# Kernel tuning notes

Hardware: AMD Instinct MI355X
Metric: run time of the kernel (lower is better)

Reference implementation:

```python
import jax, jax.numpy as jnp
import numpy as np

B, N, W = 4, 16384, 4          # batch, npoints, point feature width (xyz + intensity)
M, K = 512, 32                  # nsample keypoints, neighbors per keypoint
DIL = 2.0
NK = int(K * DIL)               # dilated candidate pool
KG = 8                          # knn size inside DGCNN edge-convs
C3 = 256


def _fps(xyz, m):
    """Farthest point sampling. xyz: (B,N,3) -> indices (B,m)."""
    Bb, Nn, _ = xyz.shape
    def step(carry, _):
        mind, cur = carry
        p = jnp.take_along_axis(xyz, cur[:, None, None], axis=1)  # (B,1,3)
        d = jnp.sum((xyz - p) ** 2, axis=-1)                       # (B,N)
        mind = jnp.minimum(mind, d)
        nxt = jnp.argmax(mind, axis=-1).astype(jnp.int32)
        return (mind, nxt), cur
    init = (jnp.full((Bb, Nn), 1e10, xyz.dtype), jnp.zeros((Bb,), jnp.int32))
    _, idx = jax.lax.scan(step, init, None, length=m)
    return jnp.transpose(idx)  # (B,m)


def _edge_conv(x, w, g, b, kg):
    """Dynamic-graph edge conv. x: (G,P,C) -> (G,P,D). Feature = cat(x_j-x_i, x_i)."""
    sq = jnp.sum(x * x, axis=-1)
    d2 = sq[:, :, None] + sq[:, None, :] - 2.0 * jnp.einsum('gpc,gqc->gpq', x, x)
    _, idx = jax.lax.top_k(-d2, kg)                                   # (G,P,kg)
    xj = jnp.take_along_axis(x[:, None], idx[..., None], axis=2)      # (G,P,kg,C)
    ef = jnp.concatenate([xj - x[:, :, None, :],
                          jnp.broadcast_to(x[:, :, None, :], xj.shape)], axis=-1)
    h = jnp.einsum('gpkc,cd->gpkd', ef, w)
    h = jax.nn.relu(g * h + b)  # BN (inference, unit running stats) + ReLU
    return jnp.max(h, axis=2)   # max over graph neighbors


def setup_inputs() -> dict:
    key = jax.random.key(0)
    ks = jax.random.split(key, 12)
    s = 0.05
    inp = {
        'x': jax.random.normal(ks[0], (B, N, W), jnp.float32),
        'rand_idx': jax.random.randint(ks[1], (K,), 0, NK),
        # DGCNN edge-conv params
        'w_e1': jax.random.normal(ks[2], (24, 64), jnp.float32) * s,
        'g1': jnp.ones((64,), jnp.float32), 'b1': jnp.zeros((64,), jnp.float32),
        'w_e2': jax.random.normal(ks[3], (128, C3), jnp.float32) * s,
        'g2': jnp.ones((C3,), jnp.float32), 'b2': jnp.zeros((C3,), jnp.float32),
        # saliency MLP (1x1 conv1d stacks)
        'w_m1': jax.random.normal(ks[4], (C3, C3), jnp.float32) * s,
        'bm1': jnp.zeros((C3,), jnp.float32),
        'gm1': jnp.ones((C3,), jnp.float32), 'bbm1': jnp.zeros((C3,), jnp.float32),
        'w_m2': jax.random.normal(ks[5], (C3, C3), jnp.float32) * s,
        'bm2': jnp.zeros((C3,), jnp.float32),
        'gm2': jnp.ones((C3,), jnp.float32), 'bbm2': jnp.zeros((C3,), jnp.float32),
        'w_m3': jax.random.normal(ks[6], (C3, 1), jnp.float32) * s,
        'bm3': jnp.zeros((1,), jnp.float32),
    }
    return inp


def reference(x, rand_idx, w_e1, g1, b1, w_e2, g2, b2,
              w_m1, bm1, gm1, bbm1, w_m2, bm2, gm2, bbm2, w_m3, bm3):
    rand_idx = rand_idx.astype(jnp.int32)
    # ---- FPS keypoint sampling ----
    node_idx = _fps(x[:, :, :3], M)                                   # (B,M)
    node = jnp.take_along_axis(x, node_idx[:, :, None], axis=1)       # (B,M,W)
    # ---- random dilation encoding: nk-NN then random k of them ----
    nxyz, pxyz = node[:, :, :3], x[:, :, :3]
    d2 = (jnp.sum(nxyz * nxyz, -1)[:, :, None] + jnp.sum(pxyz * pxyz, -1)[:, None, :]
          - 2.0 * jnp.einsum('bmc,bnc->bmn', nxyz, pxyz))             # (B,M,N)
    _, nn = jax.lax.top_k(-d2, NK)                                    # (B,M,NK)
    sel = nn[:, :, rand_idx]                                          # (B,M,K)
    neigh = jnp.take_along_axis(x[:, None], sel[..., None], axis=2)   # (B,M,K,W)
    rel = neigh[..., :3] - nxyz[:, :, None, :]
    dist = jnp.linalg.norm(rel, axis=-1, keepdims=True)
    node_rep = jnp.broadcast_to(node[:, :, None, :], neigh.shape)
    cluster = jnp.concatenate([node_rep, neigh, rel, dist], axis=-1)  # (B,M,K,12)
    random_cluster = jnp.transpose(cluster, (0, 3, 1, 2))             # (B,12,M,K)
    random_xyz = neigh[..., :3]                                       # (B,M,K,3)
    # ---- DGCNN embedding per cluster ----
    g = cluster.reshape(B * M, K, 12)
    h = _edge_conv(g, w_e1, g1, b1, KG)                               # (BM,K,64)
    h = _edge_conv(h, w_e2, g2, b2, KG)                               # (BM,K,256)
    emb = jnp.transpose(h.reshape(B, M, K, C3), (0, 3, 1, 2))         # (B,256,M,K)
    # ---- attention-weighted pooling ----
    x1 = jnp.max(emb, axis=1)                                         # (B,M,K)
    aw = jax.nn.softmax(x1, axis=-1)
    keypoints = jnp.einsum('bmk,bmkc->bcm', aw, random_xyz)           # (B,3,M)
    afm = emb * aw[:, None]                                           # (B,256,M,K)
    gcf = jnp.sum(afm, axis=-1)                                       # (B,256,M)
    # ---- saliency uncertainty MLP ----
    h = jax.nn.relu(gm1[None, :, None] * (jnp.einsum('bcm,cd->bdm', gcf, w_m1)
                                          + bm1[None, :, None]) + bbm1[None, :, None])
    h = jax.nn.relu(gm2[None, :, None] * (jnp.einsum('bcm,cd->bdm', h, w_m2)
                                          + bm2[None, :, None]) + bbm2[None, :, None])
    s = jnp.einsum('bcm,cd->bdm', h, w_m3) + bm3[None, :, None]       # (B,1,M)
    sal = jax.nn.softplus(s)[:, 0, :] + 0.001                         # (B,M)
    return keypoints, sal, random_cluster, afm
```

## Files before the change

kernel.cpp:

```cpp
#include <hip/hip_runtime.h>
#include <cstdint>

#define Bn 4
#define Nn 16384
#define Mn 512
#define Kn 32

#define O_SAL 6144
#define O_RC  8192
#define O_AFM 794624

__device__ __forceinline__ unsigned fkey(float f) {
  unsigned b = __float_as_uint(f);
  return (b & 0x80000000u) ? ~b : (b | 0x80000000u);
}

__device__ __forceinline__ unsigned long long dkey(double d) {
  unsigned long long b = (unsigned long long)__double_as_longlong(d);
  return (b & 0x8000000000000000ull) ? ~b : (b | 0x8000000000000000ull);
}

__global__ __launch_bounds__(256) void sq_kernel(const float* __restrict__ x,
                                                 float* __restrict__ sqp) {
#pragma clang fp contract(off)
  int i = blockIdx.x * 256 + threadIdx.x;
  float4 v = ((const float4*)x)[i];
  float qx = v.x * v.x;
  float qy = v.y * v.y;
  float qz = v.z * v.z;
  sqp[i] = (qx + qy) + qz;
}

template <int CTRL>
__device__ __forceinline__ float dppmaxf(float v) {
  int m = __builtin_amdgcn_update_dpp(__float_as_int(v), __float_as_int(v),
                                      CTRL, 0xf, 0xf, false);
  return fmaxf(v, __int_as_float(m));
}

__global__ __launch_bounds__(1024)
__attribute__((amdgpu_waves_per_eu(4, 4)))
void fps_kernel(const float* __restrict__ x, float* __restrict__ node) {
#pragma clang fp contract(off)
  const int b = blockIdx.x;
  const int t = threadIdx.x;
  const float4* xb = (const float4*)(x + (size_t)b * Nn * 4);
  float px[16], py[16], pz[16], mind[16];
  const int base = t * 16;
#pragma unroll
  for (int i = 0; i < 16; ++i) {
    float4 v = xb[base + i];
    px[i] = v.x; py[i] = v.y; pz[i] = v.z;
    mind[i] = 1e10f;
  }
  __shared__ __align__(16) unsigned long long kkey[2][16];
  float cx, cy, cz;
  {
    float4 v = xb[0];
    cx = v.x; cy = v.y; cz = v.z;
    if (t == 0) ((float4*)node)[b * Mn] = v;
  }
  for (int s = 1; s < Mn; ++s) {
#pragma unroll
    for (int i = 0; i < 16; ++i) {
      float dx = px[i] - cx;
      float dy = py[i] - cy;
      float dz = pz[i] - cz;
      float qx = dx * dx;
      float qy = dy * dy;
      float qz = dz * dz;
      float d = (qx + qy) + qz;
      mind[i] = fminf(mind[i], d);
    }
    float a0 = fmaxf(mind[0], mind[1]);
    float a1 = fmaxf(mind[2], mind[3]);
    float a2 = fmaxf(mind[4], mind[5]);
    float a3 = fmaxf(mind[6], mind[7]);
    float a4 = fmaxf(mind[8], mind[9]);
    float a5 = fmaxf(mind[10], mind[11]);
    float a6 = fmaxf(mind[12], mind[13]);
    float a7 = fmaxf(mind[14], mind[15]);
    float b0 = fmaxf(a0, a1);
    float b1 = fmaxf(a2, a3);
    float b2 = fmaxf(a4, a5);
    float b3 = fmaxf(a6, a7);
    float bv = fmaxf(fmaxf(b0, b1), fmaxf(b2, b3));
    int isel = 0;
#pragma unroll
    for (int i = 15; i >= 0; --i)
      if (mind[i] == bv) isel = i;
    float r = bv;
    r = dppmaxf<0x111>(r);
    r = dppmaxf<0x112>(r);
    r = dppmaxf<0x114>(r);
    r = dppmaxf<0x118>(r);
    r = dppmaxf<0x142>(r);
    r = dppmaxf<0x143>(r);
    float wmax = __int_as_float(__builtin_amdgcn_readlane(__float_as_int(r), 63));
    unsigned long long ball = __ballot(bv == wmax);
    int wl = __ffsll(ball) - 1;
    int widx = __builtin_amdgcn_readlane(base + isel, wl);
    if ((t & 63) == 0) {
      kkey[s & 1][t >> 6] =
          ((unsigned long long)(__float_as_uint(wmax) | 0x80000000u) << 32) |
          (unsigned)(~widx);
    }
    __syncthreads();
    {
      unsigned long long kk = kkey[s & 1][t & 15];
#pragma unroll
      for (int off = 1; off < 16; off <<= 1) {
        unsigned long long ok = __shfl_xor(kk, off, 16);
        kk = ok > kk ? ok : kk;
      }
      int wi = __builtin_amdgcn_readfirstlane((int)(~(unsigned)(kk & 0xFFFFFFFFu)));
      float4 nv = xb[wi];
      cx = nv.x; cy = nv.y; cz = nv.z;
      if (t == 0) ((float4*)node)[b * Mn + s] = nv;
    }
  }
}

__global__ __launch_bounds__(256) void knn_kernel(const float* __restrict__ x,
                                                  const float* __restrict__ node,
                                                  const float* __restrict__ sqp,
                                                  const int* __restrict__ rand_idx,
                                                  int* __restrict__ sel) {
#pragma clang fp contract(off)
  const int bm = blockIdx.x;
  const int b = bm >> 9;
  const int t = threadIdx.x;
  const float4* xb = (const float4*)(x + (size_t)b * Nn * 4);
  const float* sq_b = sqp + b * Nn;
  float4 nd = ((const float4*)node)[bm];
  const float nx = nd.x, ny = nd.y, nz = nd.z;
  const float sqmf = (nx * nx + ny * ny) + nz * nz;
  unsigned key[64];
#pragma unroll
  for (int i = 0; i < 64; ++i) {
    int n = t + (i << 8);
    float4 v = xb[n];
    float dot = nx * v.x;
    dot = __builtin_fmaf(ny, v.y, dot);
    dot = __builtin_fmaf(nz, v.z, dot);
    float d2 = (sqmf + sq_b[n]) - 2.0f * dot;
    key[i] = fkey(d2);
  }
  __shared__ unsigned hist[256];
  __shared__ unsigned gsum[16];
  __shared__ unsigned sh_prefix;
  __shared__ int sh_r;
  unsigned prefix = 0, pmask = 0;
  int r = 95;
  for (int shift = 24; shift >= 0; shift -= 8) {
    hist[t] = 0;
    __syncthreads();
#pragma unroll
    for (int i = 0; i < 64; ++i) {
      if ((key[i] & pmask) == prefix) atomicAdd(&hist[(key[i] >> shift) & 255], 1u);
    }
    __syncthreads();
    if (t < 16) {
      unsigned ssum = 0;
#pragma unroll
      for (int j = 0; j < 16; ++j) ssum += hist[t * 16 + j];
      gsum[t] = ssum;
    }
    __syncthreads();
    if (t == 0) {
      int rr = r;
      unsigned g = 0;
      for (unsigned j = 0; j < 16; ++j) {
        int c = (int)gsum[j];
        if (rr < c) { g = j; break; }
        rr -= c;
      }
      unsigned bin = g * 16;
      for (unsigned j = 0; j < 16; ++j) {
        int c = (int)hist[g * 16 + j];
        if (rr < c) { bin = g * 16 + j; break; }
        rr -= c;
      }
      sh_prefix = prefix | (bin << shift);
      sh_r = rr;
    }
    __syncthreads();
    prefix = sh_prefix;
    r = sh_r;
    pmask |= (0xFFu << shift);
  }
  const unsigned T = prefix;
  __shared__ int cnt;
  __shared__ unsigned long long karr[128];
  if (t == 0) cnt = 0;
  __syncthreads();
#pragma unroll
  for (int i = 0; i < 64; ++i) {
    if (key[i] <= T) {
      int pos = atomicAdd(&cnt, 1);
      if (pos < 128) {
        unsigned n = (unsigned)(t + (i << 8));
        karr[pos] = ((unsigned long long)key[i] << 32) | n;
      }
    }
  }
  __syncthreads();
  const int nc = cnt < 128 ? cnt : 128;
  if (t < 128 && t >= nc) karr[t] = ~0ull;
  for (int k = 2; k <= 128; k <<= 1) {
    for (int j = k >> 1; j > 0; j >>= 1) {
      __syncthreads();
      if (t < 64) {
        int i = ((t & ~(j - 1)) << 1) | (t & (j - 1));
        int ip = i | j;
        unsigned long long ka = karr[i], kb = karr[ip];
        bool asc = ((i & k) == 0);
        if ((ka > kb) == asc) { karr[i] = kb; karr[ip] = ka; }
      }
    }
  }
  __syncthreads();
  if (t < 32) {
    int ri = rand_idx[t];
    sel[bm * 32 + t] = (int)(unsigned)(karr[ri] & 0xFFFFFFFFu);
  }
}

__global__ __launch_bounds__(256) void group_kernel(
    const float* __restrict__ x, const float* __restrict__ node,
    const int* __restrict__ sel, const float* __restrict__ w_e1,
    const float* __restrict__ g1, const float* __restrict__ b1,
    const float* __restrict__ w_e2, const float* __restrict__ g2,
    const float* __restrict__ b2, float* __restrict__ out,
    float* __restrict__ gcf) {
#pragma clang fp contract(off)
  const int bm = blockIdx.x;
  const int b = bm >> 9;
  const int m = bm & 511;
  const int t = threadIdx.x;

  __shared__ float cl[32][13];
  __shared__ float h1t[64][36];
  __shared__ float h1p[32][68];
  __shared__ unsigned char nbr[32][8];
  __shared__ double sqs[32];
  __shared__ float part[4][32];
  __shared__ float aws[32];
  __shared__ union U {
    struct {
      unsigned long long keys[32][32];
      float we_a[12][64];
      float we_d[12][64];
      float a1[32][65];
      float cd1[32][65];
    } s;
    float a2[32 * 256];
  } u;

  const float4* xb = (const float4*)(x + (size_t)b * Nn * 4);
  const float4 ndv = ((const float4*)node)[bm];

  if (t < 32) {
    int n = sel[bm * 32 + t];
    float4 v = xb[n];
    float rx = v.x - ndv.x;
    float ry = v.y - ndv.y;
    float rz = v.z - ndv.z;
    float ds = (rx * rx + ry * ry) + rz * rz;
    ds = __fsqrt_rn(ds);
    cl[t][0] = ndv.x; cl[t][1] = ndv.y; cl[t][2] = ndv.z; cl[t][3] = ndv.w;
    cl[t][4] = v.x;   cl[t][5] = v.y;   cl[t][6] = v.z;   cl[t][7] = v.w;
    cl[t][8] = rx;    cl[t][9] = ry;    cl[t][10] = rz;   cl[t][11] = ds;
  }
  for (int i = t; i < 768; i += 256) {
    int row = i >> 6, d = i & 63;
    float wa = w_e1[row * 64 + d];
    float wb = w_e1[(row + 12) * 64 + d];
    u.s.we_a[row][d] = wa;
    u.s.we_d[row][d] = wb - wa;
  }
  __syncthreads();

  for (int i = t; i < 384; i += 256) {
    int c = i >> 5, p = i & 31;
    out[O_RC + (((size_t)(b * 12 + c) * 512) + m) * 32 + p] = cl[p][c];
  }
  if (t < 32) {
    double q[12];
#pragma unroll
    for (int c = 0; c < 12; ++c) {
      double cv = (double)cl[t][c];
      q[c] = cv * cv;
    }
    double s01 = q[0] + q[1];
    double s23 = q[2] + q[3];
    double s45 = q[4] + q[5];
    double s67 = q[6] + q[7];
    double s = (s01 + s23) + (s45 + s67);
    s = s + q[8];
    s = s + q[9];
    s = s + q[10];
    s = s + q[11];
    sqs[t] = s;
  }
  __syncthreads();

  {
    int p = t >> 3, q0 = (t & 7) << 2;
#pragma unroll
    for (int qq = 0; qq < 4; ++qq) {
      int q = q0 + qq;
      double dot = 0.0;
#pragma unroll
      for (int c = 0; c < 12; ++c)
        dot = dot + (double)cl[p][c] * (double)cl[q][c];
      double d2 = (sqs[p] + sqs[q]) - 2.0 * dot;
      u.s.keys[p][q] = dkey(d2);
    }
  }
  __syncthreads();

  {
    int p = t >> 3, s8 = t & 7;
    unsigned long long kq0 = u.s.keys[p][s8];
    unsigned long long kq1 = u.s.keys[p][s8 + 8];
    unsigned long long kq2 = u.s.keys[p][s8 + 16];
    unsigned long long kq3 = u.s.keys[p][s8 + 24];
    int r0 = 0, r1 = 0, r2 = 0, r3 = 0;
#pragma unroll
    for (int j = 0; j < 32; ++j) {
      int jj = (j + p) & 31;
      unsigned long long kj = u.s.keys[p][jj];
      r0 += (kj < kq0 || (kj == kq0 && jj < s8));
      r1 += (kj < kq1 || (kj == kq1 && jj < s8 + 8));
      r2 += (kj < kq2 || (kj == kq2 && jj < s8 + 16));
      r3 += (kj < kq3 || (kj == kq3 && jj < s8 + 24));
    }
    if (r0 < 8) nbr[p][r0] = (unsigned char)s8;
    if (r1 < 8) nbr[p][r1] = (unsigned char)(s8 + 8);
    if (r2 < 8) nbr[p][r2] = (unsigned char)(s8 + 16);
    if (r3 < 8) nbr[p][r3] = (unsigned char)(s8 + 24);
  }
  {
    int d = t & 63, pg = (t >> 6) << 3;
#pragma unroll
    for (int pp = 0; pp < 8; ++pp) {
      int p = pg + pp;
      float aA = 0.f, aD = 0.f;
#pragma unroll
      for (int c = 0; c < 12; ++c) {
        float xv = cl[p][c];
        aA = fmaf(xv, u.s.we_a[c][d], aA);
        aD = fmaf(xv, u.s.we_d[c][d], aD);
      }
      u.s.a1[p][d] = aA;
      u.s.cd1[p][d] = aD;
    }
  }
  __syncthreads();

  {
    int d = t & 63, pg = (t >> 6) << 3;
    float g1v = g1[d], b1v = b1[d];
#pragma unroll
    for (int pp = 0; pp < 8; ++pp) {
      int p = pg + pp;
      float cd = u.s.cd1[p][d];
      float hm = -1e30f;
#pragma unroll
      for (int k = 0; k < 8; ++k) {
        int j = nbr[p][k];
        float hv = fmaf(g1v, u.s.a1[j][d] + cd, b1v);
        hv = fmaxf(hv, 0.f);
        hm = fmaxf(hm, hv);
      }
      h1t[d][p] = hm;
      h1p[p][d] = hm;
    }
  }
  __syncthreads();

  if (t < 32) {
    double r[8];
#pragma unroll
    for (int j = 0; j < 8; ++j) {
      double hv = (double)h1p[t][j];
      r[j] = hv * hv;
    }
#pragma unroll
    for (int blk = 1; blk < 8; ++blk) {
#pragma unroll
      for (int j = 0; j < 8; ++j) {
        double hv = (double)h1p[t][blk * 8 + j];
        r[j] = r[j] + hv * hv;
      }
    }
    double s01 = r[0] + r[1];
    double s23 = r[2] + r[3];
    double s45 = r[4] + r[5];
    double s67 = r[6] + r[7];
    sqs[t] = (s01 + s23) + (s45 + s67);
  }
  __syncthreads();

  {
    int p = t >> 3, q0 = (t & 7) << 2;
    const float4* rp = (const float4*)&h1p[p][0];
    for (int qq = 0; qq < 4; ++qq) {
      int q = q0 + qq;
      const float4* rq = (const float4*)&h1p[q][0];
      double dot = 0.0;
#pragma unroll
      for (int c4 = 0; c4 < 16; ++c4) {
        float4 av = rp[c4];
        float4 bv = rq[c4];
        dot = dot + (double)av.x * (double)bv.x;
        dot = dot + (double)av.y * (double)bv.y;
        dot = dot + (double)av.z * (double)bv.z;
        dot = dot + (double)av.w * (double)bv.w;
      }
      double d2 = (sqs[p] + sqs[q]) - 2.0 * dot;
      u.s.keys[p][q] = dkey(d2);
    }
  }
  __syncthreads();

  {
    int p = t >> 3, s8 = t & 7;
    unsigned long long kq0 = u.s.keys[p][s8];
    unsigned long long kq1 = u.s.keys[p][s8 + 8];
    unsigned long long kq2 = u.s.keys[p][s8 + 16];
    unsigned long long kq3 = u.s.keys[p][s8 + 24];
    int r0 = 0, r1 = 0, r2 = 0, r3 = 0;
#pragma unroll
    for (int j = 0; j < 32; ++j) {
      int jj = (j + p) & 31;
      unsigned long long kj = u.s.keys[p][jj];
      r0 += (kj < kq0 || (kj == kq0 && jj < s8));
      r1 += (kj < kq1 || (kj == kq1 && jj < s8 + 8));
      r2 += (kj < kq2 || (kj == kq2 && jj < s8 + 16));
      r3 += (kj < kq3 || (kj == kq3 && jj < s8 + 24));
    }
    if (r0 < 8) nbr[p][r0] = (unsigned char)s8;
    if (r1 < 8) nbr[p][r1] = (unsigned char)(s8 + 8);
    if (r2 < 8) nbr[p][r2] = (unsigned char)(s8 + 16);
    if (r3 < 8) nbr[p][r3] = (unsigned char)(s8 + 24);
  }
  __syncthreads();

  float accD[32];
  float embv[32];
  {
    float accA[32];
#pragma unroll
    for (int p = 0; p < 32; ++p) { accA[p] = 0.f; accD[p] = 0.f; }
    for (int c = 0; c < 64; ++c) {
      float wt = w_e2[c * 256 + t];
      float wb = w_e2[(c + 64) * 256 + t];
      float wd = wb - wt;
      const float4* row = (const float4*)&h1t[c][0];
#pragma unroll
      for (int p4 = 0; p4 < 8; ++p4) {
        float4 hv = row[p4];
        accA[4 * p4 + 0] = fmaf(hv.x, wt, accA[4 * p4 + 0]);
        accA[4 * p4 + 1] = fmaf(hv.y, wt, accA[4 * p4 + 1]);
        accA[4 * p4 + 2] = fmaf(hv.z, wt, accA[4 * p4 + 2]);
        accA[4 * p4 + 3] = fmaf(hv.w, wt, accA[4 * p4 + 3]);
        accD[4 * p4 + 0] = fmaf(hv.x, wd, accD[4 * p4 + 0]);
        accD[4 * p4 + 1] = fmaf(hv.y, wd, accD[4 * p4 + 1]);
        accD[4 * p4 + 2] = fmaf(hv.z, wd, accD[4 * p4 + 2]);
        accD[4 * p4 + 3] = fmaf(hv.w, wd, accD[4 * p4 + 3]);
      }
    }
#pragma unroll
    for (int p = 0; p < 32; ++p) u.a2[p * 256 + t] = accA[p];
  }
  __syncthreads();
  {
    float g2v = g2[t], b2v = b2[t];
#pragma unroll
    for (int p = 0; p < 32; ++p) {
      float cd = accD[p];
      float e = -1e30f;
#pragma unroll
      for (int k = 0; k < 8; ++k) {
        int j = nbr[p][k];
        float hv = fmaf(g2v, u.a2[j * 256 + t] + cd, b2v);
        hv = fmaxf(hv, 0.f);
        e = fmaxf(e, hv);
      }
      embv[p] = e;
    }
  }

#pragma unroll
  for (int p = 0; p < 32; ++p) {
    float v = embv[p];
#pragma unroll
    for (int off = 32; off > 0; off >>= 1) v = fmaxf(v, __shfl_xor(v, off));
    if ((t & 63) == 0) part[t >> 6][p] = v;
  }
  __syncthreads();

  if (t < 32) {
    float x1 = fmaxf(fmaxf(part[0][t], part[1][t]), fmaxf(part[2][t], part[3][t]));
    float mx = x1;
#pragma unroll
    for (int off = 16; off > 0; off >>= 1) mx = fmaxf(mx, __shfl_xor(mx, off));
    float ex = expf(x1 - mx);
    float sm = ex;
#pragma unroll
    for (int off = 16; off > 0; off >>= 1) sm += __shfl_xor(sm, off);
    float aw = ex / sm;
    aws[t] = aw;
#pragma unroll
    for (int c = 0; c < 3; ++c) {
      float kv = aw * cl[t][4 + c];
#pragma unroll
      for (int off = 16; off > 0; off >>= 1) kv += __shfl_xor(kv, off);
      if (t == 0) out[((size_t)(b * 3 + c)) * 512 + m] = kv;
    }
  }
  __syncthreads();

  {
    float gsum = 0.f;
    size_t abase = (size_t)O_AFM + (((size_t)(b * 256 + t)) * 512 + m) * 32;
    float4* ap = (float4*)(out + abase);
#pragma unroll
    for (int p4 = 0; p4 < 8; ++p4) {
      float4 o;
      o.x = embv[4 * p4 + 0] * aws[4 * p4 + 0];
      o.y = embv[4 * p4 + 1] * aws[4 * p4 + 1];
      o.z = embv[4 * p4 + 2] * aws[4 * p4 + 2];
      o.w = embv[4 * p4 + 3] * aws[4 * p4 + 3];
      gsum += o.x; gsum += o.y; gsum += o.z; gsum += o.w;
      ap[p4] = o;
    }
    gcf[((size_t)(b * 256 + t)) * 512 + m] = gsum;
  }
}

__global__ __launch_bounds__(256) void mlp_kernel(
    const float* __restrict__ gcf, const float* __restrict__ w_m1,
    const float* __restrict__ bm1, const float* __restrict__ gm1,
    const float* __restrict__ bbm1, const float* __restrict__ w_m2,
    const float* __restrict__ bm2, const float* __restrict__ gm2,
    const float* __restrict__ bbm2, const float* __restrict__ w_m3,
    const float* __restrict__ bm3, float* __restrict__ out) {
  const int blk = blockIdx.x;
  const int b = blk >> 4;
  const int m0 = (blk & 15) << 5;
  const int t = threadIdx.x;
  __shared__ float sbuf[256 * 36];

#pragma unroll
  for (int i = 0; i < 32; ++i) {
    int c = (t >> 5) + (i << 3);
    int j = t & 31;
    sbuf[c * 36 + j] = gcf[((size_t)(b * 256 + c)) * 512 + m0 + j];
  }
  __syncthreads();

  float acc[32];
#pragma unroll
  for (int j = 0; j < 32; ++j) acc[j] = 0.f;
  for (int c = 0; c < 256; ++c) {
    float wv = w_m1[c * 256 + t];
    const float4* row = (const float4*)&sbuf[c * 36];
#pragma unroll
    for (int j4 = 0; j4 < 8; ++j4) {
      float4 g4 = row[j4];
      acc[4 * j4 + 0] = fmaf(g4.x, wv, acc[4 * j4 + 0]);
      acc[4 * j4 + 1] = fmaf(g4.y, wv, acc[4 * j4 + 1]);
      acc[4 * j4 + 2] = fmaf(g4.z, wv, acc[4 * j4 + 2]);
      acc[4 * j4 + 3] = fmaf(g4.w, wv, acc[4 * j4 + 3]);
    }
  }
  float y[32];
  {
    float gv = gm1[t], bv = bm1[t], bbv = bbm1[t];
#pragma unroll
    for (int j = 0; j < 32; ++j) y[j] = fmaxf(fmaf(gv, acc[j] + bv, bbv), 0.f);
  }
  __syncthreads();
#pragma unroll
  for (int j = 0; j < 32; ++j) sbuf[t * 36 + j] = y[j];
  __syncthreads();

#pragma unroll
  for (int j = 0; j < 32; ++j) acc[j] = 0.f;
  for (int c = 0; c < 256; ++c) {
    float wv = w_m2[c * 256 + t];
    const float4* row = (const float4*)&sbuf[c * 36];
#pragma unroll
    for (int j4 = 0; j4 < 8; ++j4) {
      float4 g4 = row[j4];
      acc[4 * j4 + 0] = fmaf(g4.x, wv, acc[4 * j4 + 0]);
      acc[4 * j4 + 1] = fmaf(g4.y, wv, acc[4 * j4 + 1]);
      acc[4 * j4 + 2] = fmaf(g4.z, wv, acc[4 * j4 + 2]);
      acc[4 * j4 + 3] = fmaf(g4.w, wv, acc[4 * j4 + 3]);
    }
  }
  {
    float gv = gm2[t], bv = bm2[t], bbv = bbm2[t];
#pragma unroll
    for (int j = 0; j < 32; ++j) y[j] = fmaxf(fmaf(gv, acc[j] + bv, bbv), 0.f);
  }
  __syncthreads();
  {
    float w3v = w_m3[t];
#pragma unroll
    for (int j = 0; j < 32; ++j) sbuf[t * 36 + j] = y[j] * w3v;
  }
  __syncthreads();
  if (t < 32) {
    float s = 0.f;
    for (int d = 0; d < 256; ++d) s += sbuf[d * 36 + t];
    s += bm3[0];
    float sal = log1pf(expf(-fabsf(s))) + fmaxf(s, 0.f) + 0.001f;
    out[O_SAL + (size_t)b * 512 + m0 + t] = sal;
  }
}

extern "C" void kernel_launch(void* const* d_in, const int* in_sizes, int n_in,
                              void* d_out, int out_size, void* d_ws, size_t ws_size,
                              hipStream_t stream) {
  (void)in_sizes; (void)n_in; (void)out_size; (void)ws_size;
  const float* x = (const float*)d_in[0];
  const int* rand_idx = (const int*)d_in[1];
  const float* w_e1 = (const float*)d_in[2];
  const float* g1 = (const float*)d_in[3];
  const float* b1 = (const float*)d_in[4];
  const float* w_e2 = (const float*)d_in[5];
  const float* g2 = (const float*)d_in[6];
  const float* b2 = (const float*)d_in[7];
  const float* w_m1 = (const float*)d_in[8];
  const float* bm1 = (const float*)d_in[9];
  const float* gm1 = (const float*)d_in[10];
  const float* bbm1 = (const float*)d_in[11];
  const float* w_m2 = (const float*)d_in[12];
  const float* bm2 = (const float*)d_in[13];
  const float* gm2 = (const float*)d_in[14];
  const float* bbm2 = (const float*)d_in[15];
  const float* w_m3 = (const float*)d_in[16];
  const float* bm3 = (const float*)d_in[17];
  float* out = (float*)d_out;
  char* ws = (char*)d_ws;

  float* node = (float*)ws;
  float* sqp = (float*)(ws + 32768);
  int* sel = (int*)(ws + 32768 + 262144);
  float* gcf = (float*)(ws + 32768 + 262144 + 262144);

  sq_kernel<<<256, 256, 0, stream>>>(x, sqp);
  fps_kernel<<<Bn, 1024, 0, stream>>>(x, node);
  knn_kernel<<<Bn * Mn, 256, 0, stream>>>(x, node, sqp, rand_idx, sel);
  group_kernel<<<Bn * Mn, 256, 0, stream>>>(x, node, sel, w_e1, g1, b1, w_e2,
                                            g2, b2, out, gcf);
  mlp_kernel<<<64, 256, 0, stream>>>(gcf, w_m1, bm1, gm1, bbm1, w_m2, bm2, gm2,
                                     bbm2, w_m3, bm3, out);
}
```

Before: 1.551 ms.

## Fuse FPS and KNN into a persistent kernel with flag-based producer-consumer overlap

Merges the sequential farthest-point-sampling kernel and the KNN selection kernel into one 512-block launch. Blocks 0-3 run FPS and publish progress every 8 sampled points through release-stored flags. The remaining blocks poll those flags with acquire loads, then run radix-select KNN for each newly ready keypoint. The goal is to hide KNN behind the long serial FPS loop and drop a kernel launch. The cost is spin-waiting, a dependence on the FPS blocks actually being resident so the pollers cannot deadlock, flags that alias the gcf workspace, and an added topk8 helper that nothing calls.

```diff
diff --git a/kernel.cpp b/kernel.cpp
--- a/kernel.cpp
+++ b/kernel.cpp
@@ -21,9 +21,11 @@
 }
 
 __global__ __launch_bounds__(256) void sq_kernel(const float* __restrict__ x,
-                                                 float* __restrict__ sqp) {
+                                                 float* __restrict__ sqp,
+                                                 unsigned long long* __restrict__ flags) {
 #pragma clang fp contract(off)
   int i = blockIdx.x * 256 + threadIdx.x;
+  if (blockIdx.x == 0 && threadIdx.x < 4) flags[threadIdx.x * 8] = 0ull;
   float4 v = ((const float4*)x)[i];
   float qx = v.x * v.x;
   float qy = v.y * v.y;
@@ -40,190 +42,228 @@
 
 __global__ __launch_bounds__(1024)
 __attribute__((amdgpu_waves_per_eu(4, 4)))
-void fps_kernel(const float* __restrict__ x, float* __restrict__ node) {
+void fused_fps_knn(const float* __restrict__ x, float* __restrict__ node,
+                   const float* __restrict__ sqp,
+                   const int* __restrict__ rand_idx, int* __restrict__ sel,
+                   unsigned long long* __restrict__ flags) {
 #pragma clang fp contract(off)
-  const int b = blockIdx.x;
   const int t = threadIdx.x;
-  const float4* xb = (const float4*)(x + (size_t)b * Nn * 4);
-  float px[16], py[16], pz[16], mind[16];
-  const int base = t * 16;
-#pragma unroll
-  for (int i = 0; i < 16; ++i) {
-    float4 v = xb[base + i];
-    px[i] = v.x; py[i] = v.y; pz[i] = v.z;
-    mind[i] = 1e10f;
-  }
   __shared__ __align__(16) unsigned long long kkey[2][16];
-  float cx, cy, cz;
-  {
-    float4 v = xb[0];
-    cx = v.x; cy = v.y; cz = v.z;
-    if (t == 0) ((float4*)node)[b * Mn] = v;
-  }
-  for (int s = 1; s < Mn; ++s) {
-#pragma unroll
-    for (int i = 0; i < 16; ++i) {
-      float dx = px[i] - cx;
-      float dy = py[i] - cy;
-      float dz = pz[i] - cz;
-      float qx = dx * dx;
-      float qy = dy * dy;
-      float qz = dz * dz;
-      float d = (qx + qy) + qz;
-      mind[i] = fminf(mind[i], d);
-    }
-    float a0 = fmaxf(mind[0], mind[1]);
-    float a1 = fmaxf(mind[2], mind[3]);
-    float a2 = fmaxf(mind[4], mind[5]);
-    float a3 = fmaxf(mind[6], mind[7]);
-    float a4 = fmaxf(mind[8], mind[9]);
-    float a5 = fmaxf(mind[10], mind[11]);
-    float a6 = fmaxf(mind[12], mind[13]);
-    float a7 = fmaxf(mind[14], mind[15]);
-    float b0 = fmaxf(a0, a1);
-    float b1 = fmaxf(a2, a3);
-    float b2 = fmaxf(a4, a5);
-    float b3 = fmaxf(a6, a7);
-    float bv = fmaxf(fmaxf(b0, b1), fmaxf(b2, b3));
-    int isel = 0;
-#pragma unroll
-    for (int i = 15; i >= 0; --i)
-      if (mind[i] == bv) isel = i;
-    float r = bv;
-    r = dppmaxf<0x111>(r);
-    r = dppmaxf<0x112>(r);
-    r = dppmaxf<0x114>(r);
-    r = dppmaxf<0x118>(r);
-    r = dppmaxf<0x142>(r);
-    r = dppmaxf<0x143>(r);
-    float wmax = __int_as_float(__builtin_amdgcn_readlane(__float_as_int(r), 63));
-    unsigned long long ball = __ballot(bv == wmax);
-    int wl = __ffsll(ball) - 1;
-    int widx = __builtin_amdgcn_readlane(base + isel, wl);
-    if ((t & 63) == 0) {
-      kkey[s & 1][t >> 6] =
-          ((unsigned long long)(__float_as_uint(wmax) | 0x80000000u) << 32) |
-          (unsigned)(~widx);
-    }
-    __syncthreads();
-    {
-      unsigned long long kk = kkey[s & 1][t & 15];
-#pragma unroll
-      for (int off = 1; off < 16; off <<= 1) {
-        unsigned long long ok = __shfl_xor(kk, off, 16);
-        kk = ok > kk ? ok : kk;
-      }
-      int wi = __builtin_amdgcn_readfirstlane((int)(~(unsigned)(kk & 0xFFFFFFFFu)));
-      float4 nv = xb[wi];
-      cx = nv.x; cy = nv.y; cz = nv.z;
-      if (t == 0) ((float4*)node)[b * Mn + s] = nv;
-    }
-  }
-}
-
-__global__ __launch_bounds__(256) void knn_kernel(const float* __restrict__ x,
-                                                  const float* __restrict__ node,
-                                                  const float* __restrict__ sqp,
-                                                  const int* __restrict__ rand_idx,
-                                                  int* __restrict__ sel) {
-#pragma clang fp contract(off)
-  const int bm = blockIdx.x;
-  const int b = bm >> 9;
-  const int t = threadIdx.x;
-  const float4* xb = (const float4*)(x + (size_t)b * Nn * 4);
-  const float* sq_b = sqp + b * Nn;
-  float4 nd = ((const float4*)node)[bm];
-  const float nx = nd.x, ny = nd.y, nz = nd.z;
-  const float sqmf = (nx * nx + ny * ny) + nz * nz;
-  unsigned key[64];
-#pragma unroll
-  for (int i = 0; i < 64; ++i) {
-    int n = t + (i << 8);
-    float4 v = xb[n];
-    float dot = nx * v.x;
-    dot = __builtin_fmaf(ny, v.y, dot);
-    dot = __builtin_fmaf(nz, v.z, dot);
-    float d2 = (sqmf + sq_b[n]) - 2.0f * dot;
-    key[i] = fkey(d2);
-  }
   __shared__ unsigned hist[256];
   __shared__ unsigned gsum[16];
   __shared__ unsigned sh_prefix;
   __shared__ int sh_r;
-  unsigned prefix = 0, pmask = 0;
-  int r = 95;
-  for (int shift = 24; shift >= 0; shift -= 8) {
-    hist[t] = 0;
-    __syncthreads();
-#pragma unroll
-    for (int i = 0; i < 64; ++i) {
-      if ((key[i] & pmask) == prefix) atomicAdd(&hist[(key[i] >> shift) & 255], 1u);
-    }
-    __syncthreads();
-    if (t < 16) {
-      unsigned ssum = 0;
-#pragma unroll
-      for (int j = 0; j < 16; ++j) ssum += hist[t * 16 + j];
-      gsum[t] = ssum;
-    }
-    __syncthreads();
-    if (t == 0) {
-      int rr = r;
-      unsigned g = 0;
-      for (unsigned j = 0; j < 16; ++j) {
-        int c = (int)gsum[j];
-        if (rr < c) { g = j; break; }
-        rr -= c;
-      }
-      unsigned bin = g * 16;
-      for (unsigned j = 0; j < 16; ++j) {
-        int c = (int)hist[g * 16 + j];
-        if (rr < c) { bin = g * 16 + j; break; }
-        rr -= c;
-      }
-      sh_prefix = prefix | (bin << shift);
-      sh_r = rr;
-    }
-    __syncthreads();
-    prefix = sh_prefix;
-    r = sh_r;
-    pmask |= (0xFFu << shift);
-  }
-  const unsigned T = prefix;
   __shared__ int cnt;
   __shared__ unsigned long long karr[128];
-  if (t == 0) cnt = 0;
-  __syncthreads();
-#pragma unroll
-  for (int i = 0; i < 64; ++i) {
-    if (key[i] <= T) {
-      int pos = atomicAdd(&cnt, 1);
-      if (pos < 128) {
-        unsigned n = (unsigned)(t + (i << 8));
-        karr[pos] = ((unsigned long long)key[i] << 32) | n;
-      }
-    }
-  }
-  __syncthreads();
-  const int nc = cnt < 128 ? cnt : 128;
-  if (t < 128 && t >= nc) karr[t] = ~0ull;
-  for (int k = 2; k <= 128; k <<= 1) {
-    for (int j = k >> 1; j > 0; j >>= 1) {
+
+  if (blockIdx.x < 4) {
+    const int b = blockIdx.x;
+    const float4* xb = (const float4*)(x + (size_t)b * Nn * 4);
+    float px[16], py[16], pz[16], mind[16];
+    const int base = t * 16;
+#pragma unroll
+    for (int i = 0; i < 16; ++i) {
+      float4 v = xb[base + i];
+      px[i] = v.x; py[i] = v.y; pz[i] = v.z;
+      mind[i] = 1e10f;
+    }
+    float cx, cy, cz;
+    {
+      float4 v = xb[0];
+      cx = v.x; cy = v.y; cz = v.z;
+      if (t == 0) ((float4*)node)[b * Mn] = v;
+    }
+    for (int s = 1; s < Mn; ++s) {
+#pragma unroll
+      for (int i = 0; i < 16; ++i) {
+        float dx = px[i] - cx;
+        float dy = py[i] - cy;
+        float dz = pz[i] - cz;
+        float qx = dx * dx;
+        float qy = dy * dy;
+        float qz = dz * dz;
+        float d = (qx + qy) + qz;
+        mind[i] = fminf(mind[i], d);
+      }
+      float a0 = fmaxf(mind[0], mind[1]);
+      float a1 = fmaxf(mind[2], mind[3]);
+      float a2 = fmaxf(mind[4], mind[5]);
+      float a3 = fmaxf(mind[6], mind[7]);
+      float a4 = fmaxf(mind[8], mind[9]);
+      float a5 = fmaxf(mind[10], mind[11]);
+      float a6 = fmaxf(mind[12], mind[13]);
+      float a7 = fmaxf(mind[14], mind[15]);
+      float b0 = fmaxf(a0, a1);
+      float b1 = fmaxf(a2, a3);
+      float b2 = fmaxf(a4, a5);
+      float b3 = fmaxf(a6, a7);
+      float bv = fmaxf(fmaxf(b0, b1), fmaxf(b2, b3));
+      int isel = 0;
+#pragma unroll
+      for (int i = 15; i >= 0; --i)
+        if (mind[i] == bv) isel = i;
+      float r = bv;
+      r = dppmaxf<0x111>(r);
+      r = dppmaxf<0x112>(r);
+      r = dppmaxf<0x114>(r);
+      r = dppmaxf<0x118>(r);
+      r = dppmaxf<0x142>(r);
+      r = dppmaxf<0x143>(r);
+      float wmax = __int_as_float(__builtin_amdgcn_readlane(__float_as_int(r), 63));
+      unsigned long long ball = __ballot(bv == wmax);
+      int wl = __ffsll(ball) - 1;
+      int widx = __builtin_amdgcn_readlane(base + isel, wl);
+      if ((t & 63) == 0) {
+        kkey[s & 1][t >> 6] =
+            ((unsigned long long)(__float_as_uint(wmax) | 0x80000000u) << 32) |
+            (unsigned)(~widx);
+      }
       __syncthreads();
-      if (t < 64) {
-        int i = ((t & ~(j - 1)) << 1) | (t & (j - 1));
-        int ip = i | j;
-        unsigned long long ka = karr[i], kb = karr[ip];
-        bool asc = ((i & k) == 0);
-        if ((ka > kb) == asc) { karr[i] = kb; karr[ip] = ka; }
-      }
-    }
-  }
-  __syncthreads();
-  if (t < 32) {
-    int ri = rand_idx[t];
-    sel[bm * 32 + t] = (int)(unsigned)(karr[ri] & 0xFFFFFFFFu);
-  }
+      {
+        unsigned long long kk = kkey[s & 1][t & 15];
+#pragma unroll
+        for (int off = 1; off < 16; off <<= 1) {
+          unsigned long long ok = __shfl_xor(kk, off, 16);
+          kk = ok > kk ? ok : kk;
+        }
+        int wi = __builtin_amdgcn_readfirstlane((int)(~(unsigned)(kk & 0xFFFFFFFFu)));
+        float4 nv = xb[wi];
+        cx = nv.x; cy = nv.y; cz = nv.z;
+        if (t == 0) ((float4*)node)[b * Mn + s] = nv;
+      }
+      if (((s & 7) == 7) && t == 0) {
+        __hip_atomic_store(&flags[b * 8], (unsigned long long)((s + 1) >> 3),
+                           __ATOMIC_RELEASE, __HIP_MEMORY_SCOPE_AGENT);
+      }
+    }
+  } else {
+    const int w = blockIdx.x - 4;
+    for (int j = w; j < Bn * Mn; j += 508) {
+      const int m = j >> 2;
+      const int bb = j & 3;
+      if (t == 0) {
+        unsigned long long need = (unsigned long long)((m >> 3) + 1);
+        while (__hip_atomic_load(&flags[bb * 8], __ATOMIC_ACQUIRE,
+                                 __HIP_MEMORY_SCOPE_AGENT) < need)
+          __builtin_amdgcn_s_sleep(8);
+      }
+      __syncthreads();
+
+      const int bm = bb * Mn + m;
+      const float4* xb = (const float4*)(x + (size_t)bb * Nn * 4);
+      const float* sq_b = sqp + bb * Nn;
+      float4 nd = ((const float4*)node)[bm];
+      const float nx = nd.x, ny = nd.y, nz = nd.z;
+      const float sqmf = (nx * nx + ny * ny) + nz * nz;
+      unsigned key[16];
+#pragma unroll
+      for (int i = 0; i < 16; ++i) {
+        int n = t + (i << 10);
+        float4 v = xb[n];
+        float dot = nx * v.x;
+        dot = __builtin_fmaf(ny, v.y, dot);
+        dot = __builtin_fmaf(nz, v.z, dot);
+        float d2 = (sqmf + sq_b[n]) - 2.0f * dot;
+        key[i] = fkey(d2);
+      }
+      unsigned prefix = 0, pmask = 0;
+      int r = 95;
+      for (int shift = 24; shift >= 0; shift -= 8) {
+        if (t < 256) hist[t] = 0;
+        __syncthreads();
+#pragma unroll
+        for (int i = 0; i < 16; ++i) {
+          if ((key[i] & pmask) == prefix)
+            atomicAdd(&hist[(key[i] >> shift) & 255], 1u);
+        }
+        __syncthreads();
+        if (t < 16) {
+          unsigned ssum = 0;
+#pragma unroll
+          for (int jj = 0; jj < 16; ++jj) ssum += hist[t * 16 + jj];
+          gsum[t] = ssum;
+        }
+        __syncthreads();
+        if (t == 0) {
+          int rr = r;
+          unsigned g = 0;
+          for (unsigned jj = 0; jj < 16; ++jj) {
+            int c = (int)gsum[jj];
+            if (rr < c) { g = jj; break; }
+            rr -= c;
+          }
+          unsigned bin = g * 16;
+          for (unsigned jj = 0; jj < 16; ++jj) {
+            int c = (int)hist[g * 16 + jj];
+            if (rr < c) { bin = g * 16 + jj; break; }
+            rr -= c;
+          }
+          sh_prefix = prefix | (bin << shift);
+          sh_r = rr;
+        }
+        __syncthreads();
+        prefix = sh_prefix;
+        r = sh_r;
+        pmask |= (0xFFu << shift);
+      }
+      const unsigned T = prefix;
+      if (t == 0) cnt = 0;
+      __syncthreads();
+#pragma unroll
+      for (int i = 0; i < 16; ++i) {
+        if (key[i] <= T) {
+          int pos = atomicAdd(&cnt, 1);
+          if (pos < 128) {
+            unsigned n = (unsigned)(t + (i << 10));
+            karr[pos] = ((unsigned long long)key[i] << 32) | n;
+          }
+        }
+      }
+      __syncthreads();
+      const int nc = cnt < 128 ? cnt : 128;
+      if (t < 128 && t >= nc) karr[t] = ~0ull;
+      for (int k = 2; k <= 128; k <<= 1) {
+        for (int jj = k >> 1; jj > 0; jj >>= 1) {
+          __syncthreads();
+          if (t < 64) {
+            int i = ((t & ~(jj - 1)) << 1) | (t & (jj - 1));
+            int ip = i | jj;
+            unsigned long long ka = karr[i], kb = karr[ip];
+            bool asc = ((i & k) == 0);
+            if ((ka > kb) == asc) { karr[i] = kb; karr[ip] = ka; }
+          }
+        }
+      }
+      __syncthreads();
+      if (t < 32) {
+        int ri = rand_idx[t];
+        sel[bm * 32 + t] = (int)(unsigned)(karr[ri] & 0xFFFFFFFFu);
+      }
+      __syncthreads();
+    }
+  }
+}
+
+__device__ __forceinline__ void topk8(const unsigned long long* row, unsigned char* nb) {
+  unsigned long long bk[8];
+  unsigned char bi[8];
+#pragma unroll
+  for (int k = 0; k < 8; ++k) { bk[k] = ~0ull; bi[k] = 255; }
+  for (int q = 0; q < 32; ++q) {
+    unsigned long long kv = row[q];
+    if (kv < bk[7]) {
+      bk[7] = kv; bi[7] = (unsigned char)q;
+#pragma unroll
+      for (int k = 6; k >= 0; --k) {
+        if (bk[k + 1] < bk[k]) {
+          unsigned long long tk = bk[k]; bk[k] = bk[k + 1]; bk[k + 1] = tk;
+          unsigned char ti = bi[k]; bi[k] = bi[k + 1]; bi[k + 1] = ti;
+        }
+      }
+    }
+  }
+#pragma unroll
+  for (int k = 0; k < 8; ++k) nb[k] = bi[k];
 }
 
 __global__ __launch_bounds__(256) void group_kernel(
@@ -652,10 +692,10 @@
   float* sqp = (float*)(ws + 32768);
   int* sel = (int*)(ws + 32768 + 262144);
   float* gcf = (float*)(ws + 32768 + 262144 + 262144);
-
-  sq_kernel<<<256, 256, 0, stream>>>(x, sqp);
-  fps_kernel<<<Bn, 1024, 0, stream>>>(x, node);
-  knn_kernel<<<Bn * Mn, 256, 0, stream>>>(x, node, sqp, rand_idx, sel);
+  unsigned long long* flags = (unsigned long long*)(ws + 32768 + 262144 + 262144);
+
+  sq_kernel<<<256, 256, 0, stream>>>(x, sqp, flags);
+  fused_fps_knn<<<512, 1024, 0, stream>>>(x, node, sqp, rand_idx, sel, flags);
   group_kernel<<<Bn * Mn, 256, 0, stream>>>(x, node, sel, w_e1, g1, b1, w_e2,
                                             g2, b2, out, gcf);
   mlp_kernel<<<64, 256, 0, stream>>>(gcf, w_m1, bm1, gm1, bbm1, w_m2, bm2, gm2,
```

Result: slower. 1.817 ms (+17.1%).
